# Kernel tuning notes

Measured on AMD Instinct MI355X. Metric: run time of the kernel, lower is better.

The kernel has to match this reference:

```python
import jax, jax.numpy as jnp
import numpy as np

N_HEAD = 16
MAX_SEQ_LEN = 2048
RATIO = 1
NEG_INF = -jnp.inf


def make_alibi_bias(n_head: int, max_seq_len: int, ratio: int) -> jnp.ndarray:
    # bias[t, s] = s*ratio - t, masked to -inf where > 0 (future positions)
    s = jnp.arange(max_seq_len)[None, :] * ratio            # [1, S]
    t = jnp.arange(max_seq_len * ratio)[:, None]            # [T, 1]
    bias = (s - t).astype(jnp.float32)                      # [T, S]
    bias = jnp.where(bias > 0, NEG_INF, bias)
    # per-head slopes: cumprod of 2^(-8/n_head) -> m_i = 2^(-8*(i+1)/n_head)
    m = jnp.cumprod(jnp.full((n_head,), 2.0 ** (-8.0 / n_head), dtype=jnp.float32))
    return bias[None, :, :] * m[:, None, None]              # [H, T, S]


def setup_inputs() -> dict:
    key = jax.random.key(0)
    kq, kk, kv = jax.random.split(key, 3)
    B, T, D = 2, 2048, 1024
    return {
        "q": jax.random.normal(kq, (B, T, D), dtype=jnp.float32),
        "k": jax.random.normal(kk, (B, T, D), dtype=jnp.float32),
        "v": jax.random.normal(kv, (B, T, D), dtype=jnp.float32),
    }


def reference(q, k, v):
    B, T, D = q.shape
    S = k.shape[1]
    H = N_HEAD
    dh = D // H
    # split heads: [B, T, D] -> [B, H, T, dh]
    qh = q.reshape(B, T, H, dh).transpose(0, 2, 1, 3)
    kh = k.reshape(B, S, H, dh).transpose(0, 2, 1, 3)
    vh = v.reshape(B, S, H, dh).transpose(0, 2, 1, 3)

    scores = jnp.einsum("bhtd,bhsd->bhts", qh, kh) / jnp.sqrt(jnp.float32(dh))
    bias = make_alibi_bias(H, MAX_SEQ_LEN, RATIO)[:, -T:, -S:]  # [H, T, S]
    attn = jax.nn.softmax(scores + bias[None], axis=-1)
    out = jnp.einsum("bhts,bhsd->bhtd", attn, vh)
    # gather heads: [B, H, T, dh] -> [B, T, D]
    return out.transpose(0, 2, 1, 3).reshape(B, T, D)
```

## Files before the change

kernel.cpp:

```cpp
#include <hip/hip_runtime.h>

#define N_HEAD 16
#define DHEAD 64
#define TSEQ 2048
#define DMODEL 1024
#define BATCH 2

typedef _Float16 f16x8 __attribute__((ext_vector_type(8)));
typedef _Float16 f16x4 __attribute__((ext_vector_type(4)));
typedef _Float16 f16x2 __attribute__((ext_vector_type(2)));
typedef __fp16 fp16x2 __attribute__((ext_vector_type(2)));
typedef float f32x4 __attribute__((ext_vector_type(4)));

union F8 { f16x8 v; uint4 u; f16x2 h[4]; };
union F4 { f16x4 v; uint2 u; f16x2 h[2]; };

#if __has_builtin(__builtin_amdgcn_exp2f)
#define EXP2F(x) __builtin_amdgcn_exp2f(x)
#else
#define EXP2F(x) exp2f(x)
#endif

__device__ __forceinline__ void gload_lds16(const void* g, void* l) {
    __builtin_amdgcn_global_load_lds(
        (const __attribute__((address_space(1))) void*)g,
        (__attribute__((address_space(3))) void*)l, 16, 0, 0);
}

__device__ __forceinline__ f16x2 pk(float a, float b) {
    union { fp16x2 i; f16x2 o; } c;
    c.i = __builtin_amdgcn_cvt_pkrtz(a, b);
    return c.o;
}

__device__ __forceinline__ F8 pack8_f32(const float* p) {
    const float4 a = *(const float4*)p;
    const float4 b = *(const float4*)(p + 4);
    F8 r;
    r.h[0] = pk(a.x, a.y); r.h[1] = pk(a.z, a.w);
    r.h[2] = pk(b.x, b.y); r.h[3] = pk(b.z, b.w);
    return r;
}

__global__ __launch_bounds__(256) void prep(const float* __restrict__ K,
                                            const float* __restrict__ V,
                                            _Float16* __restrict__ Kh,
                                            _Float16* __restrict__ Vh)
{
    __shared__ float tl[64][67];
    const int bh = blockIdx.y, b = bh >> 4, h = bh & 15;
    const int s0 = blockIdx.x * 64;
    const int t = threadIdx.x;
    const int r16 = t >> 4, c4 = (t & 15) * 4;
    #pragma unroll
    for (int pass = 0; pass < 4; ++pass) {
        const int row = pass * 16 + r16;
        const size_t goff = ((size_t)(b * TSEQ + s0 + row)) * DMODEL + h * DHEAD + c4;
        const float4 fk = *(const float4*)(K + goff);
        F4 ok;
        ok.h[0] = pk(fk.x, fk.y);
        ok.h[1] = pk(fk.z, fk.w);
        *(uint2*)(Kh + (((size_t)bh * TSEQ + s0 + row) << 6) + c4) = ok.u;
        const float4 fv = *(const float4*)(V + goff);
        tl[row][c4 + 0] = fv.x; tl[row][c4 + 1] = fv.y;
        tl[row][c4 + 2] = fv.z; tl[row][c4 + 3] = fv.w;
    }
    __syncthreads();
    const int d = t >> 2, sc = (t & 3) * 16;
    F8 p0, p1;
    #pragma unroll
    for (int j = 0; j < 4; ++j) p0.h[j] = pk(tl[sc + 2 * j][d], tl[sc + 2 * j + 1][d]);
    #pragma unroll
    for (int j = 0; j < 4; ++j) p1.h[j] = pk(tl[sc + 8 + 2 * j][d], tl[sc + 9 + 2 * j][d]);
    _Float16* vo = Vh + ((size_t)bh * DHEAD + d) * TSEQ + s0 + sc;
    *(uint4*)vo = p0.u;
    *(uint4*)(vo + 8) = p1.u;
}

__global__ __launch_bounds__(256, 2) void alibi_attn(
    const float* __restrict__ Q, const _Float16* __restrict__ Kh,
    const _Float16* __restrict__ Vh, float* __restrict__ O)
{
    __shared__ __align__(16) char smem[32768];
    char* kb0 = smem;
    char* vb0 = smem + 16384;

    const int wv   = threadIdx.x >> 6;
    const int lane = threadIdx.x & 63;
    const int quad = lane >> 4;
    const int l16  = lane & 15;

    const int bh = blockIdx.x;
    const int b  = bh >> 4, h = bh & 15;
    const int qt = 31 - (int)blockIdx.y;
    const int sx = qt;

    const float LOG2E   = 1.44269504088896f;
    const float slope   = exp2f(-0.5f * (float)(h + 1));
    const float bslope2 = slope * LOG2E;
    const float sscale2 = 0.125f * LOG2E;
    const float step64  = 64.0f * bslope2;
    const float rb1 = bslope2, rb2 = 2.f * bslope2, rb3 = 3.f * bslope2;

    const float* qp  = Q + (size_t)b * TSEQ * DMODEL + (size_t)h * DHEAD;
    const char*  kpb = (const char*)(Kh + (size_t)bh * TSEQ * DHEAD);
    const char*  vpb = (const char*)(Vh + (size_t)bh * DHEAD * TSEQ);

    const int st_r  = lane >> 3;
    const int k_src = st_r * 128  + (((lane & 7) ^ st_r) * 16);
    const int v_src = st_r * 4096 + (((lane & 7) ^ st_r) * 16);

    const int koff0 = l16 * 128 + ((quad ^ (l16 & 7)) * 16);
    const int koff1 = l16 * 128 + (((quad + 4) ^ (l16 & 7)) * 16);
    const int vbase = l16 * 128 + (quad & 1) * 8;
    const int vxw   = ((wv * 2 + (quad >> 1)) ^ (l16 & 7)) * 16;

    const f32x4 zero4 = {0.f, 0.f, 0.f, 0.f};

    auto stage = [&](int t) {
        const char* kg = kpb + (size_t)t * 8192;
        const char* vg = vpb + (size_t)t * 128;
        char* kd = kb0 + (t & 1) * 8192;
        char* vd = vb0 + (t & 1) * 8192;
        #pragma unroll
        for (int c = 0; c < 2; ++c) {
            const int gr = wv * 16 + c * 8;
            gload_lds16(kg + gr * 128 + k_src, kd + gr * 128);
            gload_lds16(vg + gr * 4096 + v_src, vd + gr * 128);
        }
    };

    stage(0);

    F8 aq[4][2];
    #pragma unroll
    for (int qb = 0; qb < 4; ++qb) {
        const float* qr = qp + (size_t)(qt * 64 + qb * 16 + l16) * DMODEL + quad * 8;
        aq[qb][0] = pack8_f32(qr);
        aq[qb][1] = pack8_f32(qr + 32);
    }

    f32x4 o[4][4];
    float lp[4];
    float dbq[4];
    #pragma unroll
    for (int qb = 0; qb < 4; ++qb) {
        #pragma unroll
        for (int nt = 0; nt < 4; ++nt) o[qb][nt] = zero4;
        lp[qb] = 0.f;
        dbq[qb] = (float)(wv * 16 + quad * 4 - qt * 64 - qb * 16 - l16) * bslope2;
    }

    __syncthreads();

    for (int t = 0; t <= sx; ++t) {
        if (t < sx) stage(t + 1);
        const char* kb = kb0 + (t & 1) * 8192;
        const char* vb = vb0 + (t & 1) * 8192;

        F8 kA0, kA1;
        kA0.u = *(const uint4*)(kb + wv * 2048 + koff0);
        kA1.u = *(const uint4*)(kb + wv * 2048 + koff1);

        F4 vf[4];
        #pragma unroll
        for (int nt = 0; nt < 4; ++nt)
            vf[nt].u = *(const uint2*)(vb + nt * 2048 + vbase + vxw);

        f32x4 sT[4];
        __builtin_amdgcn_s_setprio(1);
        #pragma unroll
        for (int qb = 0; qb < 4; ++qb) {
            f32x4 acc = zero4;
            acc = __builtin_amdgcn_mfma_f32_16x16x32_f16(kA0.v, aq[qb][0].v, acc, 0, 0, 0);
            acc = __builtin_amdgcn_mfma_f32_16x16x32_f16(kA1.v, aq[qb][1].v, acc, 0, 0, 0);
            sT[qb] = acc;
        }
        __builtin_amdgcn_s_setprio(0);

        const bool masked = (t == sx);
        F4 pP[4];
        #pragma unroll
        for (int qb = 0; qb < 4; ++qb) {
            const float db = dbq[qb];
            float p0 = EXP2F(fmaf(sT[qb][0], sscale2, db));
            float p1 = EXP2F(fmaf(sT[qb][1], sscale2, db + rb1));
            float p2 = EXP2F(fmaf(sT[qb][2], sscale2, db + rb2));
            float p3 = EXP2F(fmaf(sT[qb][3], sscale2, db + rb3));
            if (masked) {
                const int di = t * 64 + wv * 16 + quad * 4 - (qt * 64 + qb * 16 + l16);
                if (di + 0 > 0) p0 = 0.f;
                if (di + 1 > 0) p1 = 0.f;
                if (di + 2 > 0) p2 = 0.f;
                if (di + 3 > 0) p3 = 0.f;
            }
            lp[qb] += (p0 + p1) + (p2 + p3);
            pP[qb].h[0] = pk(p0, p1);
            pP[qb].h[1] = pk(p2, p3);
            dbq[qb] = db + step64;
        }

        __builtin_amdgcn_s_setprio(1);
        #pragma unroll
        for (int qb = 0; qb < 4; ++qb)
            #pragma unroll
            for (int nt = 0; nt < 4; ++nt)
                o[qb][nt] = __builtin_amdgcn_mfma_f32_16x16x16f16(
                    pP[qb].v, vf[nt].v, o[qb][nt], 0, 0, 0);
        __builtin_amdgcn_s_setprio(0);

        __syncthreads();
    }

    float lsq[4];
    #pragma unroll
    for (int qb = 0; qb < 4; ++qb) {
        float ls = lp[qb];
        ls += __shfl_xor(ls, 16);
        ls += __shfl_xor(ls, 32);
        lsq[qb] = ls;
    }
    float* lred = (float*)smem;
    if (quad == 0) {
        #pragma unroll
        for (int qb = 0; qb < 4; ++qb)
            lred[wv * 64 + qb * 16 + l16] = lsq[qb];
    }
    __syncthreads();

    const int tt   = threadIdx.x;
    const int qb2  = tt >> 7;
    const int qrow = (tt >> 3) & 15;
    const int chnk = tt & 7;
    float lA = 0.f, lB = 0.f;
    #pragma unroll
    for (int w = 0; w < 4; ++w) {
        lA += lred[w * 64 + qb2 * 16 + qrow];
        lB += lred[w * 64 + (2 + qb2) * 16 + qrow];
    }
    __syncthreads();

    float* part = (float*)smem;
    #pragma unroll
    for (int R = 0; R < 2; ++R) {
        #pragma unroll
        for (int q2 = 0; q2 < 2; ++q2) {
            const int qb = R * 2 + q2;
            #pragma unroll
            for (int nt = 0; nt < 4; ++nt) {
                const int cd = nt * 2 + (l16 >> 3);
                #pragma unroll
                for (int r = 0; r < 4; ++r) {
                    const int q  = quad * 4 + r;
                    const int cs = cd ^ (q & 7);
                    part[((wv * 2 + q2) * 16 + q) * 64 + cs * 8 + (l16 & 7)] =
                        o[qb][nt][r];
                }
            }
        }
        __syncthreads();

        const float lf = R ? lB : lA;
        const int cs = chnk ^ (qrow & 7);
        float r0[8] = {0, 0, 0, 0, 0, 0, 0, 0};
        #pragma unroll
        for (int w = 0; w < 4; ++w) {
            const float* pp = &part[((w * 2 + qb2) * 16 + qrow) * 64 + cs * 8];
            const float4 a = *(const float4*)pp;
            const float4 c = *(const float4*)(pp + 4);
            r0[0] += a.x; r0[1] += a.y; r0[2] += a.z; r0[3] += a.w;
            r0[4] += c.x; r0[5] += c.y; r0[6] += c.z; r0[7] += c.w;
        }
        const int qg = qt * 64 + (R * 2 + qb2) * 16 + qrow;
        float* op = O + ((size_t)b * TSEQ + qg) * DMODEL + h * DHEAD + chnk * 8;
        const float inv = 1.f / lf;
        float4 w0 = {r0[0] * inv, r0[1] * inv, r0[2] * inv, r0[3] * inv};
        float4 w1 = {r0[4] * inv, r0[5] * inv, r0[6] * inv, r0[7] * inv};
        *(float4*)op = w0;
        *(float4*)(op + 4) = w1;
        __syncthreads();
    }
}

extern "C" void kernel_launch(void* const* d_in, const int* in_sizes, int n_in,
                              void* d_out, int out_size, void* d_ws, size_t ws_size,
                              hipStream_t stream) {
    const float* q = (const float*)d_in[0];
    const float* k = (const float*)d_in[1];
    const float* v = (const float*)d_in[2];
    float* out = (float*)d_out;

    _Float16* Kh = (_Float16*)d_ws;
    _Float16* Vh = Kh + (size_t)BATCH * N_HEAD * TSEQ * DHEAD;

    prep<<<dim3(TSEQ / 64, BATCH * N_HEAD), 256, 0, stream>>>(k, v, Kh, Vh);
    alibi_attn<<<dim3(BATCH * N_HEAD, 32), 256, 0, stream>>>(q, Kh, Vh, out);
}
```

Measured before the change: 127.9 us.

## Use 128-row query tiles with 8 waves sharing K/V stages and balanced causal pairing

Each block now processes 128 query rows with 512 threads. Two half-groups of 4 waves share every staged K/V tile, which halves the global and LDS staging traffic per query row. Blocks are remapped so that heads pair short and long causal tiles (qt and 15-qt) within blockIdx groups, to balance the triangular workload. This costs 64KB of shared memory and more masking work on the last two tiles, and occupancy may drop because of the larger block and LDS footprint.

```diff
diff --git a/kernel.cpp b/kernel.cpp
--- a/kernel.cpp
+++ b/kernel.cpp
@@ -77,23 +77,28 @@
     *(uint4*)(vo + 8) = p1.u;
 }
 
-__global__ __launch_bounds__(256, 2) void alibi_attn(
+__global__ __launch_bounds__(512, 4) void alibi_attn(
     const float* __restrict__ Q, const _Float16* __restrict__ Kh,
     const _Float16* __restrict__ Vh, float* __restrict__ O)
 {
-    __shared__ __align__(16) char smem[32768];
+    __shared__ __align__(16) char smem[65536];
     char* kb0 = smem;
     char* vb0 = smem + 16384;
 
     const int wv   = threadIdx.x >> 6;
+    const int hf   = wv >> 2;
+    const int sw   = wv & 3;
     const int lane = threadIdx.x & 63;
     const int quad = lane >> 4;
     const int l16  = lane & 15;
 
-    const int bh = blockIdx.x;
+    const int y  = blockIdx.y;
+    const int a2 = y >> 5, r2 = y & 31, m2 = r2 >> 1, e2 = r2 & 1;
+    const int qt = (a2 ^ e2) ? (15 - m2) : m2;
+    const int bh = (int)blockIdx.x * 4 + a2 * 2 + e2;
     const int b  = bh >> 4, h = bh & 15;
-    const int qt = 31 - (int)blockIdx.y;
-    const int sx = qt;
+    const int sx = 2 * qt + 1;
+    const int dt = 2 * qt + hf;
 
     const float LOG2E   = 1.44269504088896f;
     const float slope   = exp2f(-0.5f * (float)(h + 1));
@@ -113,21 +118,19 @@
     const int koff0 = l16 * 128 + ((quad ^ (l16 & 7)) * 16);
     const int koff1 = l16 * 128 + (((quad + 4) ^ (l16 & 7)) * 16);
     const int vbase = l16 * 128 + (quad & 1) * 8;
-    const int vxw   = ((wv * 2 + (quad >> 1)) ^ (l16 & 7)) * 16;
+    const int vxw   = ((sw * 2 + (quad >> 1)) ^ (l16 & 7)) * 16;
 
     const f32x4 zero4 = {0.f, 0.f, 0.f, 0.f};
+    const int qrow0 = qt * 128 + hf * 64;
 
     auto stage = [&](int t) {
         const char* kg = kpb + (size_t)t * 8192;
         const char* vg = vpb + (size_t)t * 128;
         char* kd = kb0 + (t & 1) * 8192;
         char* vd = vb0 + (t & 1) * 8192;
-        #pragma unroll
-        for (int c = 0; c < 2; ++c) {
-            const int gr = wv * 16 + c * 8;
-            gload_lds16(kg + gr * 128 + k_src, kd + gr * 128);
-            gload_lds16(vg + gr * 4096 + v_src, vd + gr * 128);
-        }
+        const int gr = wv * 8;
+        gload_lds16(kg + gr * 128 + k_src, kd + gr * 128);
+        gload_lds16(vg + gr * 4096 + v_src, vd + gr * 128);
     };
 
     stage(0);
@@ -135,7 +138,7 @@
     F8 aq[4][2];
     #pragma unroll
     for (int qb = 0; qb < 4; ++qb) {
-        const float* qr = qp + (size_t)(qt * 64 + qb * 16 + l16) * DMODEL + quad * 8;
+        const float* qr = qp + (size_t)(qrow0 + qb * 16 + l16) * DMODEL + quad * 8;
         aq[qb][0] = pack8_f32(qr);
         aq[qb][1] = pack8_f32(qr + 32);
     }
@@ -148,7 +151,7 @@
         #pragma unroll
         for (int nt = 0; nt < 4; ++nt) o[qb][nt] = zero4;
         lp[qb] = 0.f;
-        dbq[qb] = (float)(wv * 16 + quad * 4 - qt * 64 - qb * 16 - l16) * bslope2;
+        dbq[qb] = (float)(sw * 16 + quad * 4 - (qrow0 + qb * 16 + l16)) * bslope2;
     }
 
     __syncthreads();
@@ -159,8 +162,8 @@
         const char* vb = vb0 + (t & 1) * 8192;
 
         F8 kA0, kA1;
-        kA0.u = *(const uint4*)(kb + wv * 2048 + koff0);
-        kA1.u = *(const uint4*)(kb + wv * 2048 + koff1);
+        kA0.u = *(const uint4*)(kb + sw * 2048 + koff0);
+        kA1.u = *(const uint4*)(kb + sw * 2048 + koff1);
 
         F4 vf[4];
         #pragma unroll
@@ -178,7 +181,7 @@
         }
         __builtin_amdgcn_s_setprio(0);
 
-        const bool masked = (t == sx);
+        const bool masked = (t >= dt);
         F4 pP[4];
         #pragma unroll
         for (int qb = 0; qb < 4; ++qb) {
@@ -188,7 +191,7 @@
             float p2 = EXP2F(fmaf(sT[qb][2], sscale2, db + rb2));
             float p3 = EXP2F(fmaf(sT[qb][3], sscale2, db + rb3));
             if (masked) {
-                const int di = t * 64 + wv * 16 + quad * 4 - (qt * 64 + qb * 16 + l16);
+                const int di = t * 64 + sw * 16 + quad * 4 - (qrow0 + qb * 16 + l16);
                 if (di + 0 > 0) p0 = 0.f;
                 if (di + 1 > 0) p1 = 0.f;
                 if (di + 2 > 0) p2 = 0.f;
@@ -224,23 +227,25 @@
     if (quad == 0) {
         #pragma unroll
         for (int qb = 0; qb < 4; ++qb)
-            lred[wv * 64 + qb * 16 + l16] = lsq[qb];
+            lred[(hf * 4 + sw) * 64 + qb * 16 + l16] = lsq[qb];
     }
     __syncthreads();
 
     const int tt   = threadIdx.x;
-    const int qb2  = tt >> 7;
+    const int hf2  = tt >> 8;
+    const int qb2  = (tt >> 7) & 1;
     const int qrow = (tt >> 3) & 15;
     const int chnk = tt & 7;
     float lA = 0.f, lB = 0.f;
     #pragma unroll
     for (int w = 0; w < 4; ++w) {
-        lA += lred[w * 64 + qb2 * 16 + qrow];
-        lB += lred[w * 64 + (2 + qb2) * 16 + qrow];
+        lA += lred[(hf2 * 4 + w) * 64 + qb2 * 16 + qrow];
+        lB += lred[(hf2 * 4 + w) * 64 + (2 + qb2) * 16 + qrow];
     }
     __syncthreads();
 
-    float* part = (float*)smem;
+    float* part = (float*)(smem + hf * 32768);
+    const float* partr = (const float*)(smem + hf2 * 32768);
     #pragma unroll
     for (int R = 0; R < 2; ++R) {
         #pragma unroll
@@ -253,7 +258,7 @@
                 for (int r = 0; r < 4; ++r) {
                     const int q  = quad * 4 + r;
                     const int cs = cd ^ (q & 7);
-                    part[((wv * 2 + q2) * 16 + q) * 64 + cs * 8 + (l16 & 7)] =
+                    part[((sw * 2 + q2) * 16 + q) * 64 + cs * 8 + (l16 & 7)] =
                         o[qb][nt][r];
                 }
             }
@@ -265,13 +270,13 @@
         float r0[8] = {0, 0, 0, 0, 0, 0, 0, 0};
         #pragma unroll
         for (int w = 0; w < 4; ++w) {
-            const float* pp = &part[((w * 2 + qb2) * 16 + qrow) * 64 + cs * 8];
+            const float* pp = partr + ((w * 2 + qb2) * 16 + qrow) * 64 + cs * 8;
             const float4 a = *(const float4*)pp;
             const float4 c = *(const float4*)(pp + 4);
             r0[0] += a.x; r0[1] += a.y; r0[2] += a.z; r0[3] += a.w;
             r0[4] += c.x; r0[5] += c.y; r0[6] += c.z; r0[7] += c.w;
         }
-        const int qg = qt * 64 + (R * 2 + qb2) * 16 + qrow;
+        const int qg = qt * 128 + hf2 * 64 + (R * 2 + qb2) * 16 + qrow;
         float* op = O + ((size_t)b * TSEQ + qg) * DMODEL + h * DHEAD + chnk * 8;
         const float inv = 1.f / lf;
         float4 w0 = {r0[0] * inv, r0[1] * inv, r0[2] * inv, r0[3] * inv};
@@ -294,5 +299,5 @@
     _Float16* Vh = Kh + (size_t)BATCH * N_HEAD * TSEQ * DHEAD;
 
     prep<<<dim3(TSEQ / 64, BATCH * N_HEAD), 256, 0, stream>>>(k, v, Kh, Vh);
-    alibi_attn<<<dim3(BATCH * N_HEAD, 32), 256, 0, stream>>>(q, Kh, Vh, out);
-}
+    alibi_attn<<<dim3(8, 64), 512, 0, stream>>>(q, Kh, Vh, out);
+}
```

After: 184.0 us. 1.44x slower.

## Replace LDS-staged K/V tiles with direct per-wave global loads double-buffered in registers

Applied to the files above, without the earlier changes.

Removes the shared-memory double buffer filled with global_load_lds and the per-tile __syncthreads. Each wave now reads its own K and V fragments straight from global memory into registers, with a two-stage register ping-pong that prefetches the next tile while the current one is computed. The launch bound drops the min-blocks-per-SM hint so the compiler has room for the extra registers. The intent is to avoid LDS round-trips and block-wide barriers. The cost is uncoalesced, strided global reads (V rows sit TSEQ apart), more register pressure and possibly lower occupancy.

```diff
diff --git a/kernel.cpp b/kernel.cpp
--- a/kernel.cpp
+++ b/kernel.cpp
@@ -20,12 +20,6 @@
 #else
 #define EXP2F(x) exp2f(x)
 #endif
-
-__device__ __forceinline__ void gload_lds16(const void* g, void* l) {
-    __builtin_amdgcn_global_load_lds(
-        (const __attribute__((address_space(1))) void*)g,
-        (__attribute__((address_space(3))) void*)l, 16, 0, 0);
-}
 
 __device__ __forceinline__ f16x2 pk(float a, float b) {
     union { fp16x2 i; f16x2 o; } c;
@@ -77,13 +71,11 @@
     *(uint4*)(vo + 8) = p1.u;
 }
 
-__global__ __launch_bounds__(256, 2) void alibi_attn(
+__global__ __launch_bounds__(256) void alibi_attn(
     const float* __restrict__ Q, const _Float16* __restrict__ Kh,
     const _Float16* __restrict__ Vh, float* __restrict__ O)
 {
     __shared__ __align__(16) char smem[32768];
-    char* kb0 = smem;
-    char* vb0 = smem + 16384;
 
     const int wv   = threadIdx.x >> 6;
     const int lane = threadIdx.x & 63;
@@ -102,35 +94,14 @@
     const float step64  = 64.0f * bslope2;
     const float rb1 = bslope2, rb2 = 2.f * bslope2, rb3 = 3.f * bslope2;
 
-    const float* qp  = Q + (size_t)b * TSEQ * DMODEL + (size_t)h * DHEAD;
-    const char*  kpb = (const char*)(Kh + (size_t)bh * TSEQ * DHEAD);
-    const char*  vpb = (const char*)(Vh + (size_t)bh * DHEAD * TSEQ);
-
-    const int st_r  = lane >> 3;
-    const int k_src = st_r * 128  + (((lane & 7) ^ st_r) * 16);
-    const int v_src = st_r * 4096 + (((lane & 7) ^ st_r) * 16);
-
-    const int koff0 = l16 * 128 + ((quad ^ (l16 & 7)) * 16);
-    const int koff1 = l16 * 128 + (((quad + 4) ^ (l16 & 7)) * 16);
-    const int vbase = l16 * 128 + (quad & 1) * 8;
-    const int vxw   = ((wv * 2 + (quad >> 1)) ^ (l16 & 7)) * 16;
+    const float* qp = Q + (size_t)b * TSEQ * DMODEL + (size_t)h * DHEAD;
+
+    const _Float16* kptr = Kh + (size_t)bh * TSEQ * DHEAD
+                         + (size_t)(wv * 16 + l16) * DHEAD + quad * 8;
+    const _Float16* vptr = Vh + (size_t)bh * DHEAD * TSEQ
+                         + (size_t)l16 * TSEQ + wv * 16 + quad * 4;
 
     const f32x4 zero4 = {0.f, 0.f, 0.f, 0.f};
-
-    auto stage = [&](int t) {
-        const char* kg = kpb + (size_t)t * 8192;
-        const char* vg = vpb + (size_t)t * 128;
-        char* kd = kb0 + (t & 1) * 8192;
-        char* vd = vb0 + (t & 1) * 8192;
-        #pragma unroll
-        for (int c = 0; c < 2; ++c) {
-            const int gr = wv * 16 + c * 8;
-            gload_lds16(kg + gr * 128 + k_src, kd + gr * 128);
-            gload_lds16(vg + gr * 4096 + v_src, vd + gr * 128);
-        }
-    };
-
-    stage(0);
 
     F8 aq[4][2];
     #pragma unroll
@@ -151,22 +122,19 @@
         dbq[qb] = (float)(wv * 16 + quad * 4 - qt * 64 - qb * 16 - l16) * bslope2;
     }
 
-    __syncthreads();
-
-    for (int t = 0; t <= sx; ++t) {
-        if (t < sx) stage(t + 1);
-        const char* kb = kb0 + (t & 1) * 8192;
-        const char* vb = vb0 + (t & 1) * 8192;
-
-        F8 kA0, kA1;
-        kA0.u = *(const uint4*)(kb + wv * 2048 + koff0);
-        kA1.u = *(const uint4*)(kb + wv * 2048 + koff1);
-
-        F4 vf[4];
+    auto loadK = [&](int t, F8& a0, F8& a1) {
+        const _Float16* p = kptr + (size_t)t * (64 * DHEAD);
+        a0.u = *(const uint4*)p;
+        a1.u = *(const uint4*)(p + 32);
+    };
+    auto loadV = [&](int t, F4* vf) {
+        const _Float16* p = vptr + t * 64;
         #pragma unroll
         for (int nt = 0; nt < 4; ++nt)
-            vf[nt].u = *(const uint2*)(vb + nt * 2048 + vbase + vxw);
-
+            vf[nt].u = *(const uint2*)(p + (size_t)nt * 16 * TSEQ);
+    };
+
+    auto compute = [&](int t, const F8& kA0, const F8& kA1, const F4* vf) {
         f32x4 sT[4];
         __builtin_amdgcn_s_setprio(1);
         #pragma unroll
@@ -208,8 +176,21 @@
                 o[qb][nt] = __builtin_amdgcn_mfma_f32_16x16x16f16(
                     pP[qb].v, vf[nt].v, o[qb][nt], 0, 0, 0);
         __builtin_amdgcn_s_setprio(0);
-
-        __syncthreads();
+    };
+
+    F8 kaA0, kaA1; F4 vA[4];
+    F8 kaB0, kaB1; F4 vB[4];
+    loadK(0, kaA0, kaA1); loadV(0, vA);
+
+    for (int t = 0; t <= sx; t += 2) {
+        const int t1 = (t + 1 <= sx) ? t + 1 : sx;
+        loadK(t1, kaB0, kaB1); loadV(t1, vB);
+        compute(t, kaA0, kaA1, vA);
+        if (t + 1 <= sx) {
+            const int t2 = (t + 2 <= sx) ? t + 2 : sx;
+            loadK(t2, kaA0, kaA1); loadV(t2, vA);
+            compute(t + 1, kaB0, kaB1, vB);
+        }
     }
 
     float lsq[4];
```

New measurement: 151.9 us. 1.19x slower.
